# Kernel tuning notes

Hardware: AMD Instinct MI355X
Metric: run time of the kernel (lower is better)

The kernel has to match this reference:

```python
import jax, jax.numpy as jnp
import numpy as np

N, E, IN_DIM, HID, OUT = 50000, 800000, 500, 128, 64
NUM_NA, NUM_SC, NUM_LA = 5, 2, 3


def setup_inputs() -> dict:
    key = jax.random.key(0)
    ks = jax.random.split(key, 24)
    def nrm(k, shape, scale=0.05):
        return jax.random.normal(k, shape, dtype=jnp.float32) * scale
    return {
        "x": jax.random.normal(ks[0], (N, IN_DIM), dtype=jnp.float32),
        "edge_index": jax.random.randint(ks[1], (2, E), 0, N, dtype=jnp.int32),
        "lin1_w": nrm(ks[2], (IN_DIM, HID)),
        "lin1_b": jnp.zeros((HID,), jnp.float32),
        "gcn_w": nrm(ks[3], (3, HID, HID)),
        "sage_mean_w1": nrm(ks[4], (3, HID, HID)),
        "sage_mean_w2": nrm(ks[5], (3, HID, HID)),
        "sage_max_w1": nrm(ks[6], (3, HID, HID)),
        "sage_max_w2": nrm(ks[7], (3, HID, HID)),
        "gin_w": nrm(ks[8], (3, HID, HID)),
        "gat_w": nrm(ks[9], (3, HID, HID)),
        "gat_a": nrm(ks[10], (3, 2, HID)),
        "la_max_w": nrm(ks[11], (HID, HID)),
        "la_concat_w": nrm(ks[12], (3 * HID, HID)),
        "la_mean_w": nrm(ks[13], (HID, HID)),
        "clf_w": nrm(ks[14], (HID, OUT)),
        "clf_b": jnp.zeros((OUT,), jnp.float32),
        "na_alphas": 0.001 * jax.random.normal(ks[15], (3, NUM_NA), dtype=jnp.float32),
        "sc_alphas": 0.001 * jax.random.normal(ks[16], (2, NUM_SC), dtype=jnp.float32),
        "la_alphas": 0.001 * jax.random.normal(ks[17], (1, NUM_LA), dtype=jnp.float32),
    }


def reference(x, edge_index, lin1_w, lin1_b, gcn_w, sage_mean_w1, sage_mean_w2,
              sage_max_w1, sage_max_w2, gin_w, gat_w, gat_a,
              la_max_w, la_concat_w, la_mean_w, clf_w, clf_b,
              na_alphas, sc_alphas, la_alphas):
    src, dst = edge_index[0], edge_index[1]
    seg_sum = lambda v: jax.ops.segment_sum(v, dst, num_segments=N)
    seg_max = lambda v: jax.ops.segment_max(v, dst, num_segments=N)

    ones_e = jnp.ones((E,), x.dtype)
    cnt = seg_sum(ones_e)                       # in-degree per node
    inv_cnt = 1.0 / jnp.maximum(cnt, 1.0)
    deg = cnt + 1.0                             # +1 self loop (gcn)
    norm = jax.lax.rsqrt(deg[src] * deg[dst])   # symmetric gcn norm per edge
    inv_deg = 1.0 / deg

    def na_mixed(h, i):
        # gcn
        hg = h @ gcn_w[i]
        o_gcn = seg_sum(norm[:, None] * hg[src]) + hg * inv_deg[:, None]
        # sage (mean aggregator)
        mean_agg = seg_sum(h[src]) * inv_cnt[:, None]
        o_sm = h @ sage_mean_w1[i] + mean_agg @ sage_mean_w2[i]
        # sage (max aggregator)
        mx = seg_max(h[src])
        mx = jnp.where(jnp.isfinite(mx), mx, 0.0)
        o_sx = h @ sage_max_w1[i] + mx @ sage_max_w2[i]
        # gin (eps = 0)
        o_gin = (h + seg_sum(h[src])) @ gin_w[i]
        # gat (single head, segment softmax over incoming edges)
        hw = h @ gat_w[i]
        e_src = hw @ gat_a[i, 0]
        e_dst = hw @ gat_a[i, 1]
        e = jax.nn.leaky_relu(e_src[src] + e_dst[dst], 0.2)
        emax = seg_max(e)
        emax = jnp.where(jnp.isfinite(emax), emax, 0.0)
        ee = jnp.exp(e - emax[dst])
        denom = seg_sum(ee)
        coef = ee / (denom[dst] + 1e-16)
        o_gat = seg_sum(coef[:, None] * hw[src])
        w = jax.nn.softmax(na_alphas[i])        # [5]
        stack = jnp.stack([o_gcn, o_sm, o_sx, o_gin, o_gat])  # [5, N, H]
        return jnp.einsum('k,knh->nh', w, jax.nn.elu(stack))

    # dropout is identity (eval mode)
    h0 = x @ lin1_w + lin1_b
    x1 = na_mixed(h0, 0)
    x2 = na_mixed(x1, 1)
    x3 = na_mixed(x2, 2)

    # SC mixed: SC_PRIMITIVES = [none, skip] -> w_none*0 + w_skip*x
    sc_w = jax.nn.softmax(sc_alphas, axis=-1)   # [2, 2]
    s1 = sc_w[0, 1] * x1
    s2 = sc_w[1, 1] * x2

    # LA mixed over (x3, s1, s2): [l_max, l_concat, l_mean], each w * relu(op)
    la_w = jax.nn.softmax(la_alphas, axis=-1)[0]  # [3]
    xs = jnp.stack([x3, s1, s2])                   # [3, N, H]
    o_max = jax.nn.relu(jnp.max(xs, axis=0) @ la_max_w)
    o_cat = jax.nn.relu(jnp.concatenate([x3, s1, s2], axis=-1) @ la_concat_w)
    o_mean = jax.nn.relu(jnp.mean(xs, axis=0) @ la_mean_w)
    x5 = la_w[0] * o_max + la_w[1] * o_cat + la_w[2] * o_mean

    return x5 @ clf_w + clf_b
```

## Files before the change

kernel.cpp:

```cpp
#include <hip/hip_runtime.h>
#include <math.h>

#define HID 128
#define IN_DIM_C 500

__device__ inline float eluf(float x) { return x > 0.f ? x : expm1f(x); }

__global__ void prep_kernel(const float* __restrict__ na, const float* __restrict__ sc,
                            const float* __restrict__ la, float* __restrict__ s) {
    if (threadIdx.x != 0 || blockIdx.x != 0) return;
    for (int i = 0; i < 3; ++i) {
        float m = -1e30f;
        for (int k = 0; k < 5; ++k) m = fmaxf(m, na[i * 5 + k]);
        float d = 0.f;
        for (int k = 0; k < 5; ++k) d += expf(na[i * 5 + k] - m);
        for (int k = 0; k < 5; ++k) s[i * 5 + k] = expf(na[i * 5 + k] - m) / d;
    }
    for (int i = 0; i < 2; ++i) {
        float a = sc[i * 2], b = sc[i * 2 + 1];
        float m = fmaxf(a, b);
        float e0 = expf(a - m), e1 = expf(b - m);
        s[15 + i] = e1 / (e0 + e1);
    }
    {
        float m = fmaxf(la[0], fmaxf(la[1], la[2]));
        float d = 0.f;
        for (int k = 0; k < 3; ++k) d += expf(la[k] - m);
        for (int k = 0; k < 3; ++k) s[17 + k] = expf(la[k] - m) / d;
    }
}

__global__ void gatvec_kernel(const float* __restrict__ gat_w, const float* __restrict__ gat_a,
                              float* __restrict__ va) {
    int b = blockIdx.x;
    int layer = b >> 1, which = b & 1;
    int j = threadIdx.x;
    const float* W = gat_w + ((size_t)layer * HID + j) * HID;
    const float* a = gat_a + (size_t)layer * 2 * HID + which * HID;
    float s = 0.f;
    for (int k = 0; k < HID; k += 4) {
        float4 w = *(const float4*)&W[k];
        float4 av = *(const float4*)&a[k];
        s += w.x * av.x + w.y * av.y + w.z * av.z + w.w * av.w;
    }
    va[b * HID + j] = s;
}

__global__ void zero_int_kernel(int* __restrict__ p, int n) {
    int i = blockIdx.x * blockDim.x + threadIdx.x;
    if (i < n) p[i] = 0;
}

__global__ void degree_kernel(const int* __restrict__ dst, int* __restrict__ cnt, int E) {
    int e = blockIdx.x * blockDim.x + threadIdx.x;
    if (e < E) atomicAdd(&cnt[dst[e]], 1);
}

__global__ __launch_bounds__(1024) void exscan_kernel(const int* __restrict__ in,
                                                      int* __restrict__ out, int n) {
    __shared__ int buf[1024];
    int t = threadIdx.x;
    int chunk = (n + 1023) >> 10;
    int base = t * chunk;
    int end = base + chunk;
    if (end > n) end = n;
    int s = 0;
    for (int i = base; i < end; ++i) s += in[i];
    buf[t] = s;
    __syncthreads();
    int x = s;
    for (int o = 1; o < 1024; o <<= 1) {
        int add = (t >= o) ? buf[t - o] : 0;
        __syncthreads();
        x += add;
        buf[t] = x;
        __syncthreads();
    }
    int running = x - s;
    for (int i = base; i < end; ++i) {
        out[i] = running;
        running += in[i];
    }
}

__global__ void node_scalars_kernel(const int* __restrict__ cnt, float* __restrict__ rsqd,
                                    float* __restrict__ invcnt, float* __restrict__ invdeg, int n) {
    int i = blockIdx.x * blockDim.x + threadIdx.x;
    if (i >= n) return;
    float c = (float)cnt[i];
    rsqd[i] = rsqrtf(c + 1.f);
    invcnt[i] = 1.f / fmaxf(c, 1.f);
    invdeg[i] = 1.f / (c + 1.f);
}

__global__ void csr_fill_kernel(const int* __restrict__ src, const int* __restrict__ dst,
                                const int* __restrict__ offs, int* __restrict__ cursor,
                                int* __restrict__ csr_src, int E) {
    int e = blockIdx.x * blockDim.x + threadIdx.x;
    if (e >= E) return;
    int d = dst[e];
    int pos = offs[d] + atomicAdd(&cursor[d], 1);
    csr_src[pos] = src[e];
}

__device__ __forceinline__ void gemm_body(
    const float* A1, const float* __restrict__ B1, const float* __restrict__ sc1p,
    const float* A2, const float* __restrict__ B2, const float* __restrict__ sc2p,
    const float* A3, const float* __restrict__ B3, const float* __restrict__ sc3p,
    const float* __restrict__ bias, float* C,
    int n, int K, int ncol, int act, int blk) {
    __shared__ float As[64][64];
    __shared__ float Bs[64][128];
    const int t = threadIdx.x;
    const int tx = t & 31, ty = t >> 5;
    const int rowbase = blk * 64;

    float4 acc[8];
#pragma unroll
    for (int r = 0; r < 8; ++r) { acc[r].x = 0.f; acc[r].y = 0.f; acc[r].z = 0.f; acc[r].w = 0.f; }

    const float* Aarr[3] = {A1, A2, A3};
    const float* Barr[3] = {B1, B2, B3};
    const float* scarr[3] = {sc1p, sc2p, sc3p};

    const int nf4 = ncol >> 2;

    for (int op = 0; op < 3; ++op) {
        const float* A = Aarr[op];
        if (!A) break;
        const float* B = Barr[op];
        float scv = scarr[op] ? *scarr[op] : 1.f;
        for (int k0 = 0; k0 < K; k0 += 64) {
            __syncthreads();
#pragma unroll
            for (int i = 0; i < 4; ++i) {
                int idx = t + i * 256;
                int row = idx >> 4, f4 = idx & 15;
                int grow = rowbase + row, gk = k0 + f4 * 4;
                float4 v; v.x = v.y = v.z = v.w = 0.f;
                if (grow < n) {
                    if (gk + 4 <= K) {
                        v = *(const float4*)&A[(size_t)grow * K + gk];
                    } else {
                        float tmp[4] = {0.f, 0.f, 0.f, 0.f};
                        for (int kk = 0; kk < 4; ++kk)
                            if (gk + kk < K) tmp[kk] = A[(size_t)grow * K + gk + kk];
                        v.x = tmp[0]; v.y = tmp[1]; v.z = tmp[2]; v.w = tmp[3];
                    }
                    v.x *= scv; v.y *= scv; v.z *= scv; v.w *= scv;
                }
                *(float4*)&As[row][f4 * 4] = v;
            }
            for (int idx = t; idx < 64 * nf4; idx += 256) {
                int kr = idx / nf4, c4 = idx % nf4;
                int gk = k0 + kr;
                float4 v; v.x = v.y = v.z = v.w = 0.f;
                if (gk < K) v = *(const float4*)&B[(size_t)gk * ncol + c4 * 4];
                *(float4*)&Bs[kr][c4 * 4] = v;
            }
            __syncthreads();
            if (tx * 4 < ncol) {
                for (int k = 0; k < 64; k += 4) {
                    float4 b0 = *(const float4*)&Bs[k][tx * 4];
                    float4 b1 = *(const float4*)&Bs[k + 1][tx * 4];
                    float4 b2 = *(const float4*)&Bs[k + 2][tx * 4];
                    float4 b3 = *(const float4*)&Bs[k + 3][tx * 4];
#pragma unroll
                    for (int r = 0; r < 8; ++r) {
                        float4 a = *(const float4*)&As[ty * 8 + r][k];
                        acc[r].x += a.x * b0.x + a.y * b1.x + a.z * b2.x + a.w * b3.x;
                        acc[r].y += a.x * b0.y + a.y * b1.y + a.z * b2.y + a.w * b3.y;
                        acc[r].z += a.x * b0.z + a.y * b1.z + a.z * b2.z + a.w * b3.z;
                        acc[r].w += a.x * b0.w + a.y * b1.w + a.z * b2.w + a.w * b3.w;
                    }
                }
            }
        }
    }

    if (tx * 4 < ncol) {
        float4 bv; bv.x = bv.y = bv.z = bv.w = 0.f;
        if (bias) bv = *(const float4*)&bias[tx * 4];
#pragma unroll
        for (int r = 0; r < 8; ++r) {
            int row = rowbase + ty * 8 + r;
            if (row >= n) break;
            float4 v = acc[r];
            v.x += bv.x; v.y += bv.y; v.z += bv.z; v.w += bv.w;
            if (act) {
                v.x = fmaxf(v.x, 0.f); v.y = fmaxf(v.y, 0.f);
                v.z = fmaxf(v.z, 0.f); v.w = fmaxf(v.w, 0.f);
            }
            *(float4*)&C[(size_t)row * ncol + tx * 4] = v;
        }
    }
}

__global__ __launch_bounds__(256) void gemm_f32(
    const float* A1, const float* __restrict__ B1, const float* __restrict__ sc1p,
    const float* A2, const float* __restrict__ B2, const float* __restrict__ sc2p,
    const float* A3, const float* __restrict__ B3, const float* __restrict__ sc3p,
    const float* __restrict__ bias, float* C,
    int n, int K, int ncol, int act) {
    gemm_body(A1, B1, sc1p, A2, B2, sc2p, A3, B3, sc3p, bias, C, n, K, ncol, act,
              blockIdx.x);
}

__global__ __launch_bounds__(256) void gemm_layer5(
    const float* __restrict__ h,
    float* AGa, const float* __restrict__ Wa,
    float* AGg, const float* __restrict__ Wg,
    float* TG,  const float* __restrict__ Wgin,
    float* AGs, const float* __restrict__ Wsm1, const float* __restrict__ Wsm2,
    float* AGm, const float* __restrict__ Wsx1, const float* __restrict__ Wsx2,
    int n) {
    const float *A1 = nullptr, *B1 = nullptr, *A2 = nullptr, *B2 = nullptr;
    float* C = nullptr;
    switch (blockIdx.y) {
        case 0: A1 = AGa; B1 = Wa;   C = AGa; break;
        case 1: A1 = AGg; B1 = Wg;   C = AGg; break;
        case 2: A1 = TG;  B1 = Wgin; C = TG;  break;
        case 3: A1 = h;   B1 = Wsm1; A2 = AGs; B2 = Wsm2; C = AGs; break;
        default: A1 = h;  B1 = Wsx1; A2 = AGm; B2 = Wsx2; C = AGm; break;
    }
    gemm_body(A1, B1, nullptr, A2, B2, nullptr, nullptr, nullptr, nullptr,
              nullptr, C, n, HID, HID, 0, blockIdx.x);
}

__global__ __launch_bounds__(256) void eproj_kernel(const float* __restrict__ h,
                                                    const float* __restrict__ va, int layer,
                                                    float* __restrict__ es, float* __restrict__ ed,
                                                    int n) {
    int wid = (blockIdx.x * 256 + threadIdx.x) >> 6;
    int lane = threadIdx.x & 63;
    if (wid >= n) return;
    float2 v = *(const float2*)&h[(size_t)wid * HID + lane * 2];
    float2 w0 = *(const float2*)&va[(layer * 2 + 0) * HID + lane * 2];
    float2 w1 = *(const float2*)&va[(layer * 2 + 1) * HID + lane * 2];
    float s0 = v.x * w0.x + v.y * w0.y;
    float s1 = v.x * w1.x + v.y * w1.y;
#pragma unroll
    for (int o = 32; o > 0; o >>= 1) {
        s0 += __shfl_xor(s0, o);
        s1 += __shfl_xor(s1, o);
    }
    if (lane == 0) { es[wid] = s0; ed[wid] = s1; }
}

__global__ __launch_bounds__(256) void aggregate_kernel(
    const float* __restrict__ h, const int* __restrict__ csr_src,
    const float* __restrict__ es, const float* __restrict__ ed,
    const int* __restrict__ offs, const int* __restrict__ cnt,
    const float* __restrict__ rsqd, const float* __restrict__ invcnt,
    const float* __restrict__ invdeg,
    float* __restrict__ sm_in, float* __restrict__ gcn_in, float* __restrict__ gin_in,
    float* __restrict__ ag_max, float* __restrict__ ag_gat, int n) {
    int wid = (blockIdx.x * 256 + threadIdx.x) >> 6;
    int lane = threadIdx.x & 63;
    if (wid >= n) return;
    int beg = offs[wid];
    int m = cnt[wid];
    int end = beg + m;
    float edv = ed[wid];

    float emax = -INFINITY;
    for (int j = beg + lane; j < end; j += 64) {
        float v = es[csr_src[j]] + edv;
        float e = v > 0.f ? v : 0.2f * v;
        emax = fmaxf(emax, e);
    }
#pragma unroll
    for (int o = 32; o > 0; o >>= 1) emax = fmaxf(emax, __shfl_xor(emax, o));
    float den = 0.f;
    for (int j = beg + lane; j < end; j += 64) {
        float v = es[csr_src[j]] + edv;
        float e = v > 0.f ? v : 0.2f * v;
        den += __expf(e - emax);
    }
#pragma unroll
    for (int o = 32; o > 0; o >>= 1) den += __shfl_xor(den, o);
    float inv_den = 1.f / (den + 1e-16f);

    const float2* h2 = (const float2*)h;
    float sx = 0.f, sy = 0.f, gx = 0.f, gy = 0.f, ax = 0.f, ay = 0.f;
    float mxx = -INFINITY, mxy = -INFINITY;
#pragma unroll 4
    for (int j = beg; j < end; ++j) {
        int s = csr_src[j];
        float v = es[s] + edv;
        float e = v > 0.f ? v : 0.2f * v;
        float coef = __expf(e - emax) * inv_den;
        float rsd = rsqd[s];
        float2 hv = h2[(size_t)s * 64 + lane];
        sx += hv.x; sy += hv.y;
        gx += rsd * hv.x; gy += rsd * hv.y;
        mxx = fmaxf(mxx, hv.x); mxy = fmaxf(mxy, hv.y);
        ax += coef * hv.x; ay += coef * hv.y;
    }
    if (m == 0) { mxx = 0.f; mxy = 0.f; }

    size_t o2 = (size_t)wid * 64 + lane;
    float2 hd = h2[o2];
    float icnt = invcnt[wid];
    float idg = invdeg[wid];
    float rsd_d = rsqd[wid];
    float2 r;
    r.x = icnt * sx;             r.y = icnt * sy;             ((float2*)sm_in)[o2] = r;
    r.x = idg * hd.x + rsd_d * gx; r.y = idg * hd.y + rsd_d * gy; ((float2*)gcn_in)[o2] = r;
    r.x = hd.x + sx;             r.y = hd.y + sy;             ((float2*)gin_in)[o2] = r;
    r.x = mxx;                   r.y = mxy;                   ((float2*)ag_max)[o2] = r;
    r.x = ax;                    r.y = ay;                    ((float2*)ag_gat)[o2] = r;
}

__global__ void combine_kernel(const float* __restrict__ o_gcn, const float* __restrict__ o_sm,
                               const float* __restrict__ o_sx, const float* __restrict__ o_gin,
                               const float* __restrict__ o_gat,
                               const float* __restrict__ scal, int layer,
                               float* __restrict__ xo, int n) {
    int i = blockIdx.x * blockDim.x + threadIdx.x;
    int tot = n * 32;
    if (i >= tot) return;
    float4 g = ((const float4*)o_gcn)[i];
    float4 sm = ((const float4*)o_sm)[i];
    float4 sx = ((const float4*)o_sx)[i];
    float4 gi = ((const float4*)o_gin)[i];
    float4 ga = ((const float4*)o_gat)[i];
    float w0 = scal[layer * 5 + 0], w1 = scal[layer * 5 + 1], w2 = scal[layer * 5 + 2];
    float w3 = scal[layer * 5 + 3], w4 = scal[layer * 5 + 4];
    float4 r;
    r.x = w0 * eluf(g.x) + w1 * eluf(sm.x) + w2 * eluf(sx.x) + w3 * eluf(gi.x) + w4 * eluf(ga.x);
    r.y = w0 * eluf(g.y) + w1 * eluf(sm.y) + w2 * eluf(sx.y) + w3 * eluf(gi.y) + w4 * eluf(ga.y);
    r.z = w0 * eluf(g.z) + w1 * eluf(sm.z) + w2 * eluf(sx.z) + w3 * eluf(gi.z) + w4 * eluf(ga.z);
    r.w = w0 * eluf(g.w) + w1 * eluf(sm.w) + w2 * eluf(sx.w) + w3 * eluf(gi.w) + w4 * eluf(ga.w);
    ((float4*)xo)[i] = r;
}

__global__ void maxmean_kernel(const float* __restrict__ x1, const float* __restrict__ x2,
                               const float* __restrict__ x3, const float* __restrict__ scal,
                               float* __restrict__ omax, float* __restrict__ omean, int tot4) {
    int i = blockIdx.x * blockDim.x + threadIdx.x;
    if (i >= tot4) return;
    float s1 = scal[15], s2 = scal[16];
    float4 a = ((const float4*)x3)[i];
    float4 b = ((const float4*)x1)[i];
    float4 c = ((const float4*)x2)[i];
    b.x *= s1; b.y *= s1; b.z *= s1; b.w *= s1;
    c.x *= s2; c.y *= s2; c.z *= s2; c.w *= s2;
    float4 mx, mn;
    mx.x = fmaxf(a.x, fmaxf(b.x, c.x)); mx.y = fmaxf(a.y, fmaxf(b.y, c.y));
    mx.z = fmaxf(a.z, fmaxf(b.z, c.z)); mx.w = fmaxf(a.w, fmaxf(b.w, c.w));
    const float third = 1.f / 3.f;
    mn.x = (a.x + b.x + c.x) * third; mn.y = (a.y + b.y + c.y) * third;
    mn.z = (a.z + b.z + c.z) * third; mn.w = (a.w + b.w + c.w) * third;
    ((float4*)omax)[i] = mx;
    ((float4*)omean)[i] = mn;
}

__global__ void la_comb_kernel(const float* __restrict__ o_max, const float* __restrict__ o_cat,
                               const float* __restrict__ o_mean, const float* __restrict__ scal,
                               float* __restrict__ x5, int tot4) {
    int i = blockIdx.x * blockDim.x + threadIdx.x;
    if (i >= tot4) return;
    float l0 = scal[17], l1 = scal[18], l2 = scal[19];
    float4 a = ((const float4*)o_max)[i];
    float4 b = ((const float4*)o_cat)[i];
    float4 c = ((const float4*)o_mean)[i];
    float4 r;
    r.x = l0 * a.x + l1 * b.x + l2 * c.x;
    r.y = l0 * a.y + l1 * b.y + l2 * c.y;
    r.z = l0 * a.z + l1 * b.z + l2 * c.z;
    r.w = l0 * a.w + l1 * b.w + l2 * c.w;
    ((float4*)x5)[i] = r;
}

extern "C" void kernel_launch(void* const* d_in, const int* in_sizes, int n_in,
                              void* d_out, int out_size, void* d_ws, size_t ws_size,
                              hipStream_t stream) {
    const float* x = (const float*)d_in[0];
    const int* edge_index = (const int*)d_in[1];
    const float* lin1_w = (const float*)d_in[2];
    const float* lin1_b = (const float*)d_in[3];
    const float* gcn_w = (const float*)d_in[4];
    const float* sage_mean_w1 = (const float*)d_in[5];
    const float* sage_mean_w2 = (const float*)d_in[6];
    const float* sage_max_w1 = (const float*)d_in[7];
    const float* sage_max_w2 = (const float*)d_in[8];
    const float* gin_w = (const float*)d_in[9];
    const float* gat_w = (const float*)d_in[10];
    const float* gat_a = (const float*)d_in[11];
    const float* la_max_w = (const float*)d_in[12];
    const float* la_concat_w = (const float*)d_in[13];
    const float* la_mean_w = (const float*)d_in[14];
    const float* clf_w = (const float*)d_in[15];
    const float* clf_b = (const float*)d_in[16];
    const float* na_alphas = (const float*)d_in[17];
    const float* sc_alphas = (const float*)d_in[18];
    const float* la_alphas = (const float*)d_in[19];
    float* out = (float*)d_out;

    const int N = in_sizes[0] / IN_DIM_C;
    const int E = in_sizes[1] / 2;
    const int* src = edge_index;
    const int* dst = edge_index + E;

    char* base = (char*)d_ws;
    size_t off = 0;
    auto alloc = [&](size_t bytes) -> void* {
        void* p = base + off;
        off += (bytes + 255) & ~(size_t)255;
        return p;
    };
    const size_t NF = (size_t)N * HID * sizeof(float);
    float* S0 = (float*)alloc(NF);
    float* S1 = (float*)alloc(NF);
    float* S2 = (float*)alloc(NF);
    float* S3 = (float*)alloc(NF);
    float* AGs = (float*)alloc(NF);
    float* AGg = (float*)alloc(NF);
    float* AGm = (float*)alloc(NF);
    float* AGa = (float*)alloc(NF);
    float* TG  = (float*)alloc(NF);
    int* csr_src = (int*)alloc((size_t)E * sizeof(int));
    int* cnt_i = (int*)alloc((size_t)2 * N * sizeof(int));
    int* cursor = cnt_i + N;
    int* offs = (int*)alloc((size_t)N * sizeof(int));
    float* rsqd = (float*)alloc((size_t)N * sizeof(float));
    float* invcnt = (float*)alloc((size_t)N * sizeof(float));
    float* invdeg = (float*)alloc((size_t)N * sizeof(float));
    float* e_src_b = (float*)alloc((size_t)N * sizeof(float));
    float* e_dst_b = (float*)alloc((size_t)N * sizeof(float));
    float* va = (float*)alloc(6 * HID * sizeof(float));
    float* scal = (float*)alloc(64 * sizeof(float));

    const int NB_elem = (N * 32 + 255) / 256;
    const int NB_gemm = (N + 63) / 64;
    const int NB_edge = (E + 255) / 256;
    const int NB_wave = (N + 3) / 4;
    const int NB_node = (N + 255) / 256;

    prep_kernel<<<1, 64, 0, stream>>>(na_alphas, sc_alphas, la_alphas, scal);
    gatvec_kernel<<<6, HID, 0, stream>>>(gat_w, gat_a, va);
    zero_int_kernel<<<(2 * N + 255) / 256, 256, 0, stream>>>(cnt_i, 2 * N);
    degree_kernel<<<NB_edge, 256, 0, stream>>>(dst, cnt_i, E);
    exscan_kernel<<<1, 1024, 0, stream>>>(cnt_i, offs, N);
    node_scalars_kernel<<<NB_node, 256, 0, stream>>>(cnt_i, rsqd, invcnt, invdeg, N);
    csr_fill_kernel<<<NB_edge, 256, 0, stream>>>(src, dst, offs, cursor, csr_src, E);

    gemm_f32<<<NB_gemm, 256, 0, stream>>>(
        x, lin1_w, nullptr,
        nullptr, nullptr, nullptr,
        nullptr, nullptr, nullptr,
        lin1_b, S0, N, IN_DIM_C, HID, 0);

    const float* h = S0;
    float* xouts[3] = {S1, S2, S3};
    for (int i = 0; i < 3; ++i) {
        const float* Wg = gcn_w + (size_t)i * HID * HID;
        const float* Wa = gat_w + (size_t)i * HID * HID;
        const float* Wsm1 = sage_mean_w1 + (size_t)i * HID * HID;
        const float* Wsm2 = sage_mean_w2 + (size_t)i * HID * HID;
        const float* Wsx1 = sage_max_w1 + (size_t)i * HID * HID;
        const float* Wsx2 = sage_max_w2 + (size_t)i * HID * HID;
        const float* Wgin = gin_w + (size_t)i * HID * HID;
        float* xo = xouts[i];

        eproj_kernel<<<NB_wave, 256, 0, stream>>>(h, va, i, e_src_b, e_dst_b, N);
        aggregate_kernel<<<NB_wave, 256, 0, stream>>>(h, csr_src, e_src_b, e_dst_b,
                                                      offs, cnt_i,
                                                      rsqd, invcnt, invdeg,
                                                      AGs, AGg, TG, AGm, AGa, N);
        gemm_layer5<<<dim3(NB_gemm, 5), 256, 0, stream>>>(
            h, AGa, Wa, AGg, Wg, TG, Wgin, AGs, Wsm1, Wsm2, AGm, Wsx1, Wsx2, N);
        combine_kernel<<<NB_elem, 256, 0, stream>>>(AGg, AGs, AGm, TG, AGa, scal, i, xo, N);
        h = xo;
    }

    maxmean_kernel<<<NB_elem, 256, 0, stream>>>(S1, S2, S3, scal, AGs, AGg, N * 32);
    gemm_f32<<<NB_gemm, 256, 0, stream>>>(AGs, la_max_w, nullptr,
                                          nullptr, nullptr, nullptr,
                                          nullptr, nullptr, nullptr,
                                          nullptr, AGm, N, HID, HID, 1);
    gemm_f32<<<NB_gemm, 256, 0, stream>>>(S3, la_concat_w, nullptr,
                                          S1, la_concat_w + HID * HID, scal + 15,
                                          S2, la_concat_w + 2 * HID * HID, scal + 16,
                                          nullptr, TG, N, HID, HID, 1);
    gemm_f32<<<NB_gemm, 256, 0, stream>>>(AGg, la_mean_w, nullptr,
                                          nullptr, nullptr, nullptr,
                                          nullptr, nullptr, nullptr,
                                          nullptr, AGg, N, HID, HID, 1);
    la_comb_kernel<<<NB_elem, 256, 0, stream>>>(AGm, TG, AGg, scal, AGs, N * 32);
    gemm_f32<<<NB_gemm, 256, 0, stream>>>(AGs, clf_w, nullptr,
                                          nullptr, nullptr, nullptr,
                                          nullptr, nullptr, nullptr,
                                          clf_b, out, N, HID, 64, 0);
}
```

Measured before the change: 1.656 ms.

## Use split-bf16 MFMA for per-layer 128x128 GEMMs with prepacked weights

Replaces the FP32 SIMT GEMM for the five per-layer operator projections with a matrix-core kernel that uses bf16 MFMA 16x16x32. Each operand is split into hi and lo bf16 parts and combined with three MFMAs, which approximates FP32 accuracy. Weights are converted once into a fragment-ready packed layout by a new setup kernel, and activations are converted into swizzled LDS tiles. This trades the FP32 FMA cost for matrix-core throughput plus conversion work, and accuracy drops slightly because the lo*lo term is omitted.

```diff
diff --git a/kernel.cpp b/kernel.cpp
--- a/kernel.cpp
+++ b/kernel.cpp
@@ -4,7 +4,20 @@
 #define HID 128
 #define IN_DIM_C 500
 
+typedef __attribute__((ext_vector_type(8))) short short8v;
+typedef __attribute__((ext_vector_type(4))) short short4v;
+typedef __attribute__((ext_vector_type(4))) float f32x4;
+
 __device__ inline float eluf(float x) { return x > 0.f ? x : expm1f(x); }
+
+__device__ inline unsigned short f2bf(float x) {
+    unsigned u = __float_as_uint(x);
+    u += 0x7fff + ((u >> 16) & 1);
+    return (unsigned short)(u >> 16);
+}
+__device__ inline float bf2f(unsigned short h) {
+    return __uint_as_float(((unsigned)h) << 16);
+}
 
 __global__ void prep_kernel(const float* __restrict__ na, const float* __restrict__ sc,
                             const float* __restrict__ la, float* __restrict__ s) {
@@ -44,6 +57,41 @@
         s += w.x * av.x + w.y * av.y + w.z * av.z + w.w * av.w;
     }
     va[b * HID + j] = s;
+}
+
+__global__ void convw_kernel(const float* __restrict__ gat_w, const float* __restrict__ gcn_w,
+                             const float* __restrict__ gin_w, const float* __restrict__ sm1,
+                             const float* __restrict__ sm2, const float* __restrict__ sx1,
+                             const float* __restrict__ sx2,
+                             unsigned short* __restrict__ pk_hi,
+                             unsigned short* __restrict__ pk_lo) {
+    int tid = blockIdx.x * 256 + threadIdx.x;
+    if (tid >= 21 * 32 * 64) return;
+    int l = tid & 63;
+    int p = (tid >> 6) & 31;
+    int m = tid >> 11;
+    int op = m / 3, layer = m % 3;
+    const float* W;
+    switch (op) {
+        case 0: W = gat_w; break;
+        case 1: W = gcn_w; break;
+        case 2: W = gin_w; break;
+        case 3: W = sm1; break;
+        case 4: W = sm2; break;
+        case 5: W = sx1; break;
+        default: W = sx2; break;
+    }
+    W += (size_t)layer * HID * HID;
+    int kc = p >> 3, ct = p & 7;
+    int kbase = kc * 32 + 8 * (l >> 4);
+    int col = ct * 16 + (l & 15);
+    size_t dbase = ((size_t)m * 2048 + (size_t)p * 64 + l) * 8;
+    for (int j = 0; j < 8; ++j) {
+        float x = W[(size_t)(kbase + j) * HID + col];
+        unsigned short h = f2bf(x);
+        pk_hi[dbase + j] = h;
+        pk_lo[dbase + j] = f2bf(x - bf2f(h));
+    }
 }
 
 __global__ void zero_int_kernel(int* __restrict__ p, int n) {
@@ -206,25 +254,89 @@
               blockIdx.x);
 }
 
-__global__ __launch_bounds__(256) void gemm_layer5(
+__global__ __launch_bounds__(256) void gemm5_mfma(
     const float* __restrict__ h,
-    float* AGa, const float* __restrict__ Wa,
-    float* AGg, const float* __restrict__ Wg,
-    float* TG,  const float* __restrict__ Wgin,
-    float* AGs, const float* __restrict__ Wsm1, const float* __restrict__ Wsm2,
-    float* AGm, const float* __restrict__ Wsx1, const float* __restrict__ Wsx2,
-    int n) {
-    const float *A1 = nullptr, *B1 = nullptr, *A2 = nullptr, *B2 = nullptr;
-    float* C = nullptr;
+    float* AGa, float* AGg, float* TG, float* AGs, float* AGm,
+    const unsigned short* __restrict__ pk_hi, const unsigned short* __restrict__ pk_lo,
+    int layer, int n) {
+    __shared__ short Ah[64 * 128];
+    __shared__ short Al[64 * 128];
+    const int t = threadIdx.x;
+    const int w = t >> 6, l = t & 63;
+    const int rowbase = blockIdx.x * 64;
+
+    const float* A1; const float* A2 = nullptr; float* C;
+    int m1, m2 = -1;
     switch (blockIdx.y) {
-        case 0: A1 = AGa; B1 = Wa;   C = AGa; break;
-        case 1: A1 = AGg; B1 = Wg;   C = AGg; break;
-        case 2: A1 = TG;  B1 = Wgin; C = TG;  break;
-        case 3: A1 = h;   B1 = Wsm1; A2 = AGs; B2 = Wsm2; C = AGs; break;
-        default: A1 = h;  B1 = Wsx1; A2 = AGm; B2 = Wsx2; C = AGm; break;
-    }
-    gemm_body(A1, B1, nullptr, A2, B2, nullptr, nullptr, nullptr, nullptr,
-              nullptr, C, n, HID, HID, 0, blockIdx.x);
+        case 0: A1 = AGa; C = AGa; m1 = 0 + layer; break;
+        case 1: A1 = AGg; C = AGg; m1 = 3 + layer; break;
+        case 2: A1 = TG;  C = TG;  m1 = 6 + layer; break;
+        case 3: A1 = h; A2 = AGs; C = AGs; m1 = 9 + layer;  m2 = 12 + layer; break;
+        default: A1 = h; A2 = AGm; C = AGm; m1 = 15 + layer; m2 = 18 + layer; break;
+    }
+
+    f32x4 acc[8];
+#pragma unroll
+    for (int ct = 0; ct < 8; ++ct) { acc[ct][0] = 0.f; acc[ct][1] = 0.f; acc[ct][2] = 0.f; acc[ct][3] = 0.f; }
+
+    for (int opi = 0; opi < 2; ++opi) {
+        const float* A = opi ? A2 : A1;
+        if (!A) break;
+        int mm = opi ? m2 : m1;
+        __syncthreads();
+#pragma unroll
+        for (int i = 0; i < 8; ++i) {
+            int idx = t + i * 256;
+            int row = idx >> 5;
+            int kb = (idx & 31) * 4;
+            int grow = rowbase + row;
+            float4 v; v.x = v.y = v.z = v.w = 0.f;
+            if (grow < n) v = *(const float4*)&A[(size_t)grow * HID + kb];
+            unsigned short h0 = f2bf(v.x), h1 = f2bf(v.y), h2 = f2bf(v.z), h3 = f2bf(v.w);
+            short4v hv; hv[0] = (short)h0; hv[1] = (short)h1; hv[2] = (short)h2; hv[3] = (short)h3;
+            short4v lv;
+            lv[0] = (short)f2bf(v.x - bf2f(h0));
+            lv[1] = (short)f2bf(v.y - bf2f(h1));
+            lv[2] = (short)f2bf(v.z - bf2f(h2));
+            lv[3] = (short)f2bf(v.w - bf2f(h3));
+            int boff = row * 256 + ((kb * 2) ^ ((row & 7) << 4));
+            *(short4v*)((char*)Ah + boff) = hv;
+            *(short4v*)((char*)Al + boff) = lv;
+        }
+        __syncthreads();
+        const unsigned short* bh = pk_hi + (size_t)mm * 16384;
+        const unsigned short* bl = pk_lo + (size_t)mm * 16384;
+        const int arow = (w << 4) + (l & 15);
+        const int swz = (arow & 7) << 4;
+        const int abase = arow * 256;
+#pragma unroll
+        for (int kc = 0; kc < 4; ++kc) {
+            int k0 = kc * 32 + ((l >> 4) << 3);
+            int boffA = abase + ((k0 * 2) ^ swz);
+            short8v a_h = *(const short8v*)((const char*)Ah + boffA);
+            short8v a_l = *(const short8v*)((const char*)Al + boffA);
+#pragma unroll
+            for (int ct = 0; ct < 8; ++ct) {
+                size_t fo = (((size_t)(kc * 8 + ct)) * 64 + l) * 8;
+                short8v b_h = *(const short8v*)&bh[fo];
+                short8v b_l = *(const short8v*)&bl[fo];
+                acc[ct] = __builtin_amdgcn_mfma_f32_16x16x32_bf16(a_h, b_h, acc[ct], 0, 0, 0);
+                acc[ct] = __builtin_amdgcn_mfma_f32_16x16x32_bf16(a_l, b_h, acc[ct], 0, 0, 0);
+                acc[ct] = __builtin_amdgcn_mfma_f32_16x16x32_bf16(a_h, b_l, acc[ct], 0, 0, 0);
+            }
+        }
+    }
+
+    const int colb = l & 15;
+    const int rgrp = (l >> 4) << 2;
+#pragma unroll
+    for (int ct = 0; ct < 8; ++ct) {
+#pragma unroll
+        for (int r = 0; r < 4; ++r) {
+            int row = rowbase + (w << 4) + rgrp + r;
+            if (row < n) C[(size_t)row * HID + ct * 16 + colb] = acc[ct][r];
+        }
+    }
 }
 
 __global__ __launch_bounds__(256) void eproj_kernel(const float* __restrict__ h,
@@ -431,6 +543,8 @@
     float* e_dst_b = (float*)alloc((size_t)N * sizeof(float));
     float* va = (float*)alloc(6 * HID * sizeof(float));
     float* scal = (float*)alloc(64 * sizeof(float));
+    unsigned short* pk_hi = (unsigned short*)alloc((size_t)21 * 16384 * sizeof(unsigned short));
+    unsigned short* pk_lo = (unsigned short*)alloc((size_t)21 * 16384 * sizeof(unsigned short));
 
     const int NB_elem = (N * 32 + 255) / 256;
     const int NB_gemm = (N + 63) / 64;
@@ -440,6 +554,9 @@
 
     prep_kernel<<<1, 64, 0, stream>>>(na_alphas, sc_alphas, la_alphas, scal);
     gatvec_kernel<<<6, HID, 0, stream>>>(gat_w, gat_a, va);
+    convw_kernel<<<(21 * 32 * 64 + 255) / 256, 256, 0, stream>>>(
+        gat_w, gcn_w, gin_w, sage_mean_w1, sage_mean_w2, sage_max_w1, sage_max_w2,
+        pk_hi, pk_lo);
     zero_int_kernel<<<(2 * N + 255) / 256, 256, 0, stream>>>(cnt_i, 2 * N);
     degree_kernel<<<NB_edge, 256, 0, stream>>>(dst, cnt_i, E);
     exscan_kernel<<<1, 1024, 0, stream>>>(cnt_i, offs, N);
@@ -455,22 +572,14 @@
     const float* h = S0;
     float* xouts[3] = {S1, S2, S3};
     for (int i = 0; i < 3; ++i) {
-        const float* Wg = gcn_w + (size_t)i * HID * HID;
-        const float* Wa = gat_w + (size_t)i * HID * HID;
-        const float* Wsm1 = sage_mean_w1 + (size_t)i * HID * HID;
-        const float* Wsm2 = sage_mean_w2 + (size_t)i * HID * HID;
-        const float* Wsx1 = sage_max_w1 + (size_t)i * HID * HID;
-        const float* Wsx2 = sage_max_w2 + (size_t)i * HID * HID;
-        const float* Wgin = gin_w + (size_t)i * HID * HID;
         float* xo = xouts[i];
-
         eproj_kernel<<<NB_wave, 256, 0, stream>>>(h, va, i, e_src_b, e_dst_b, N);
         aggregate_kernel<<<NB_wave, 256, 0, stream>>>(h, csr_src, e_src_b, e_dst_b,
                                                       offs, cnt_i,
                                                       rsqd, invcnt, invdeg,
                                                       AGs, AGg, TG, AGm, AGa, N);
-        gemm_layer5<<<dim3(NB_gemm, 5), 256, 0, stream>>>(
-            h, AGa, Wa, AGg, Wg, TG, Wgin, AGs, Wsm1, Wsm2, AGm, Wsx1, Wsx2, N);
+        gemm5_mfma<<<dim3(NB_gemm, 5), 256, 0, stream>>>(
+            h, AGa, AGg, TG, AGs, AGm, pk_hi, pk_lo, i, N);
         combine_kernel<<<NB_elem, 256, 0, stream>>>(AGg, AGs, AGm, TG, AGa, scal, i, xo, N);
         h = xo;
     }
```

Result: faster. 1.552 ms (-6.3%).
